# Kernel tuning notes

Hardware: AMD Instinct MI355X
Metric: run time of the kernel (lower is better)

## Reference

```python
import jax, jax.numpy as jnp
import numpy as np

B, T, C = 4, 2048, 1024
NUM_HEADS, HEAD_DIM = 16, 64
INNER = NUM_HEADS * HEAD_DIM
OUT_DIM = 1024


def setup_inputs() -> dict:
    key = jax.random.key(0)
    kx, kk, kq, kv, kp = jax.random.split(key, 5)
    return {
        "x": jax.random.normal(kx, (B, T, C), dtype=jnp.float32),
        "W_k": jax.random.normal(kk, (INNER, C), dtype=jnp.float32),
        "W_q": jax.random.normal(kq, (INNER, C), dtype=jnp.float32),
        "W_v": jax.random.normal(kv, (INNER, C), dtype=jnp.float32),
        "W_p": jax.random.normal(kp, (OUT_DIM, INNER), dtype=jnp.float32),
    }


def reference(x, W_k, W_q, W_v, W_p):
    b, t, c = x.shape
    h, d = NUM_HEADS, HEAD_DIM
    scale_in = c ** (-0.5)
    # project and split heads: [B, H, T, D]
    def proj(W):
        y = jnp.einsum('btc,ic->bti', x, W) * scale_in
        return y.reshape(b, t, h, d).transpose(0, 2, 1, 3)
    k = proj(W_k)
    q = proj(W_q)
    v = proj(W_v)
    scores = jnp.einsum('bhqd,bhkd->bhqk', q, k) * (d ** (-0.5))
    weight = jax.nn.softmax(scores, axis=-1)
    out = jnp.einsum('bhqk,bhkd->bhqd', weight, v)  # [B,H,T,D]
    out = out.transpose(0, 2, 1, 3).reshape(b, t, h * d)
    out = jnp.einsum('bti,oi->bto', out, W_p) * (W_p.shape[-1] ** (-0.5))
    return out
```

## Files before the change

kernel.cpp:

```cpp
#include <hip/hip_runtime.h>
#include <math.h>

typedef __attribute__((ext_vector_type(8))) short bh8;
typedef __attribute__((ext_vector_type(4))) float f32x4;

namespace {
constexpr int Bn = 4, Tn = 2048, Cn = 1024, Hn = 16, Dn = 64, INNERn = 1024, OUTn = 1024;
constexpr int Mn = Bn * Tn;
}

__device__ __forceinline__ void glds16(const void* g, void* l) {
    __builtin_amdgcn_global_load_lds(
        (const __attribute__((address_space(1))) void*)g,
        (__attribute__((address_space(3))) void*)l, 16, 0, 0);
}

__device__ __forceinline__ void barrier_vm0() {
    __builtin_amdgcn_s_waitcnt(0x0070);
    __builtin_amdgcn_s_barrier();
}

__device__ __forceinline__ ushort f2bf(float f) {
    union { float f; unsigned u; } v; v.f = f;
    unsigned r = v.u + 0x7fffu + ((v.u >> 16) & 1u);
    return (ushort)(r >> 16);
}
__device__ __forceinline__ unsigned pack_rne(float a, float b) {
    return (unsigned)f2bf(a) | ((unsigned)f2bf(b) << 16);
}
__device__ __forceinline__ unsigned pack_trunc(float a, float b) {
    return __builtin_amdgcn_perm(__float_as_uint(a), __float_as_uint(b), 0x03020706u);
}

__global__ __launch_bounds__(256)
void cvt_all(const float* __restrict__ x,  const float* __restrict__ Wk,
             const float* __restrict__ Wq, const float* __restrict__ Wv,
             const float* __restrict__ Wp,
             ushort* __restrict__ xb,  ushort* __restrict__ wkb,
             ushort* __restrict__ wqb, ushort* __restrict__ wvb,
             ushort* __restrict__ wpb)
{
    const int bid = blockIdx.x;
    const float* s; ushort* d; float sc; int i;
    if (bid < 8192) {
        s = x; d = xb; sc = 0.03125f;
        i = bid * 256 + threadIdx.x;
    } else {
        const int seg = (bid - 8192) >> 10;
        i = ((bid - 8192) & 1023) * 256 + threadIdx.x;
        s  = (seg == 0) ? Wk : (seg == 1) ? Wq : (seg == 2) ? Wv : Wp;
        d  = (seg == 0) ? wkb : (seg == 1) ? wqb : (seg == 2) ? wvb : wpb;
        sc = (seg == 3) ? 0.03125f : 1.0f;
    }
    float4 f = ((const float4*)s)[i];
    ushort4 o;
    o.x = f2bf(f.x * sc); o.y = f2bf(f.y * sc);
    o.z = f2bf(f.z * sc); o.w = f2bf(f.w * sc);
    ((ushort4*)d)[i] = o;
}

__global__ __launch_bounds__(256)
void gemm_qkv(const ushort* __restrict__ A, const ushort* __restrict__ Wq,
              const ushort* __restrict__ Wk, const ushort* __restrict__ Wv,
              ushort* __restrict__ Oq, ushort* __restrict__ Ok,
              ushort* __restrict__ Ovt, float qscale)
{
    __shared__ char As[2][8192];
    __shared__ char Bs[2][8192];
    const int tid = threadIdx.x;
    const int w = tid >> 6, lane = tid & 63, quad = lane >> 4, l = lane & 15;
    const int sel = blockIdx.x >> 3;
    const ushort* Bw = (sel == 0) ? Wq : (sel == 1) ? Wk : Wv;
    const int n0 = (blockIdx.x & 7) * 128, m0 = blockIdx.y * 128;
    const int wm = w >> 1, wn = w & 1;

    auto stage = [&](int bsel, int k0) {
#pragma unroll
        for (int rr = 0; rr < 2; ++rr) {
            const int rho = w * 2 + rr;
            const int row = rho * 16 + (lane >> 2);
            const int kq  = (lane & 3) * 8;
            glds16(A  + (size_t)(m0 + row) * Cn + k0 + kq, As[bsel] + rho * 1024 + lane * 16);
            glds16(Bw + (size_t)(n0 + row) * Cn + k0 + kq, Bs[bsel] + rho * 1024 + lane * 16);
        }
    };

    f32x4 acc[4][4];
#pragma unroll
    for (int i = 0; i < 4; ++i)
#pragma unroll
        for (int j = 0; j < 4; ++j) acc[i][j] = (f32x4){0.f, 0.f, 0.f, 0.f};

    stage(0, 0);
    barrier_vm0();
#pragma unroll 2
    for (int it = 0; it < 32; ++it) {
        const int cur = it & 1;
        if (it < 31) stage(cur ^ 1, (it + 1) * 32);
        const char* Ac = As[cur]; const char* Bc = Bs[cur];
        bh8 af[4], bf[4];
#pragma unroll
        for (int mf = 0; mf < 4; ++mf)
            af[mf] = *(const bh8*)(Ac + (wm * 64 + mf * 16 + l) * 64 + quad * 16);
#pragma unroll
        for (int nf = 0; nf < 4; ++nf)
            bf[nf] = *(const bh8*)(Bc + (wn * 64 + nf * 16 + l) * 64 + quad * 16);
#pragma unroll
        for (int mf = 0; mf < 4; ++mf)
#pragma unroll
            for (int nf = 0; nf < 4; ++nf)
                acc[mf][nf] = __builtin_amdgcn_mfma_f32_16x16x32_bf16(af[mf], bf[nf], acc[mf][nf], 0, 0, 0);
        barrier_vm0();
    }

    if (sel < 2) {
        ushort* dU = (sel == 0) ? Oq : Ok;
        const float scale = (sel == 0) ? qscale : 1.0f;
#pragma unroll
        for (int mf = 0; mf < 4; ++mf)
#pragma unroll
            for (int nf = 0; nf < 4; ++nf) {
                const int mb = m0 + wm * 64 + mf * 16 + quad * 4;
                const int n  = n0 + wn * 64 + nf * 16 + l;
                const int h = n >> 6, dd = n & 63;
#pragma unroll
                for (int reg = 0; reg < 4; ++reg) {
                    const int m = mb + reg;
                    const int b = m >> 11, t = m & (Tn - 1);
                    dU[((size_t)(b * Hn + h) * Tn + t) * Dn + dd] = f2bf(acc[mf][nf][reg] * scale);
                }
            }
    } else {
#pragma unroll
        for (int mf = 0; mf < 4; ++mf)
#pragma unroll
            for (int nf = 0; nf < 4; ++nf) {
                const int mb = m0 + wm * 64 + mf * 16 + quad * 4;
                const int n  = n0 + wn * 64 + nf * 16 + l;
                const int h = n >> 6, dd = n & 63;
                const int b = mb >> 11, t0 = mb & (Tn - 1);
                uint2 p;
                p.x = pack_rne(acc[mf][nf][0], acc[mf][nf][1]);
                p.y = pack_rne(acc[mf][nf][2], acc[mf][nf][3]);
                *(uint2*)(Ovt + ((size_t)(b * Hn + h) * Dn + dd) * Tn + t0) = p;
            }
    }
}

__global__ __launch_bounds__(256)
void gemm_po(const ushort* __restrict__ A, const ushort* __restrict__ Bw,
             float* __restrict__ Cout)
{
    __shared__ char As[2][8192];
    __shared__ char Bs[2][8192];
    const int tid = threadIdx.x;
    const int w = tid >> 6, lane = tid & 63, quad = lane >> 4, l = lane & 15;
    const int n0 = blockIdx.x * 128, m0 = blockIdx.y * 128;
    const int wm = w >> 1, wn = w & 1;

    auto stage = [&](int bsel, int k0) {
#pragma unroll
        for (int rr = 0; rr < 2; ++rr) {
            const int rho = w * 2 + rr;
            const int row = rho * 16 + (lane >> 2);
            const int kq  = (lane & 3) * 8;
            glds16(A  + (size_t)(m0 + row) * Cn + k0 + kq, As[bsel] + rho * 1024 + lane * 16);
            glds16(Bw + (size_t)(n0 + row) * Cn + k0 + kq, Bs[bsel] + rho * 1024 + lane * 16);
        }
    };

    f32x4 acc[4][4];
#pragma unroll
    for (int i = 0; i < 4; ++i)
#pragma unroll
        for (int j = 0; j < 4; ++j) acc[i][j] = (f32x4){0.f, 0.f, 0.f, 0.f};

    stage(0, 0);
    barrier_vm0();
#pragma unroll 2
    for (int it = 0; it < 32; ++it) {
        const int cur = it & 1;
        if (it < 31) stage(cur ^ 1, (it + 1) * 32);
        const char* Ac = As[cur]; const char* Bc = Bs[cur];
        bh8 af[4], bf[4];
#pragma unroll
        for (int mf = 0; mf < 4; ++mf)
            af[mf] = *(const bh8*)(Ac + (wm * 64 + mf * 16 + l) * 64 + quad * 16);
#pragma unroll
        for (int nf = 0; nf < 4; ++nf)
            bf[nf] = *(const bh8*)(Bc + (wn * 64 + nf * 16 + l) * 64 + quad * 16);
#pragma unroll
        for (int mf = 0; mf < 4; ++mf)
#pragma unroll
            for (int nf = 0; nf < 4; ++nf)
                acc[mf][nf] = __builtin_amdgcn_mfma_f32_16x16x32_bf16(af[mf], bf[nf], acc[mf][nf], 0, 0, 0);
        barrier_vm0();
    }

#pragma unroll
    for (int mf = 0; mf < 4; ++mf)
#pragma unroll
        for (int nf = 0; nf < 4; ++nf) {
            const int mb = m0 + wm * 64 + mf * 16 + quad * 4;
            const int n  = n0 + wn * 64 + nf * 16 + l;
#pragma unroll
            for (int reg = 0; reg < 4; ++reg)
                Cout[(size_t)(mb + reg) * OUTn + n] = acc[mf][nf][reg];
        }
}

__global__ __launch_bounds__(256, 2)
void attn_mfma(const ushort* __restrict__ Qg, const ushort* __restrict__ Kg,
               const ushort* __restrict__ Vtg, ushort* __restrict__ Og)
{
    __shared__ char KT[2][8192];
    __shared__ char VT[2][8192];
    __shared__ char PS[16384];

    const int tid = threadIdx.x;
    const int w = tid >> 6, lane = tid & 63, quad = lane >> 4, l = lane & 15;
    const int q0 = blockIdx.x * 256;
    const int bh = blockIdx.y, b = bh >> 4, h = bh & 15;
    const ushort* Qp = Qg  + (size_t)bh * Tn * Dn;
    const ushort* Kp = Kg  + (size_t)bh * Tn * Dn;
    const ushort* Vp = Vtg + (size_t)bh * Dn * Tn;

    auto stageK = [&](char* buf, int kt) {
#pragma unroll
        for (int rr = 0; rr < 2; ++rr) {
            const int rho = w * 2 + rr;
            const int r  = (rho & 3) * 16 + (lane >> 2);
            const int dq = (rho >> 2) * 32 + (lane & 3) * 8;
            glds16(Kp + (size_t)(kt * 64 + r) * Dn + dq, buf + rho * 1024 + lane * 16);
        }
    };
    auto stageV = [&](char* buf, int kt) {
#pragma unroll
        for (int rr = 0; rr < 2; ++rr) {
            const int rho = w * 2 + rr;
            const int d = rho * 8 + (lane >> 3);
            const int csrc = (lane & 7) ^ ((lane >> 3) & 7);
            glds16(Vp + (size_t)d * Tn + kt * 64 + csrc * 8, buf + rho * 1024 + lane * 16);
        }
    };

    bh8 qf[4][2];
#pragma unroll
    for (int nt = 0; nt < 4; ++nt)
#pragma unroll
        for (int ks = 0; ks < 2; ++ks)
            qf[nt][ks] = *(const bh8*)(Qp + (size_t)(q0 + w * 64 + nt * 16 + l) * Dn + ks * 32 + quad * 8);

    bh8 ones;
#pragma unroll
    for (int i = 0; i < 8; ++i) ones[i] = (short)0x3F80;

    f32x4 oacc[4][4], lacc[4];
#pragma unroll
    for (int nt = 0; nt < 4; ++nt) {
        lacc[nt] = (f32x4){0.f, 0.f, 0.f, 0.f};
#pragma unroll
        for (int dt = 0; dt < 4; ++dt) oacc[nt][dt] = (f32x4){0.f, 0.f, 0.f, 0.f};
    }

    char* Pw = PS + w * 4096;
    const f32x4 zero = (f32x4){0.f, 0.f, 0.f, 0.f};

    stageK(KT[0], 0);
    stageV(VT[0], 0);
    barrier_vm0();

    for (int kt = 0; kt < Tn / 64; ++kt) {
        const int cur = kt & 1;
        if (kt < Tn / 64 - 1) {
            stageK(KT[cur ^ 1], kt + 1);
            stageV(VT[cur ^ 1], kt + 1);
        }
        const char* Kc = KT[cur];
        const char* Vc = VT[cur];

#pragma unroll
        for (int hh = 0; hh < 2; ++hh) {
            bh8 kf[2][2];
#pragma unroll
            for (int k8l = 0; k8l < 2; ++k8l)
#pragma unroll
                for (int ks = 0; ks < 2; ++ks)
                    kf[k8l][ks] = *(const bh8*)(Kc + ks * 4096 + ((hh * 2 + k8l) * 16 + l) * 64 + quad * 16);

            f32x4 st[4][2];
#pragma unroll
            for (int nt = 0; nt < 4; ++nt)
#pragma unroll
                for (int k8l = 0; k8l < 2; ++k8l) {
                    st[nt][k8l] = __builtin_amdgcn_mfma_f32_16x16x32_bf16(kf[k8l][0], qf[nt][0], zero, 0, 0, 0);
                    st[nt][k8l] = __builtin_amdgcn_mfma_f32_16x16x32_bf16(kf[k8l][1], qf[nt][1], st[nt][k8l], 0, 0, 0);
                }

#pragma unroll
            for (int nt = 0; nt < 4; ++nt)
#pragma unroll
                for (int k8l = 0; k8l < 2; ++k8l) {
                    const float e0 = __builtin_amdgcn_exp2f(st[nt][k8l][0]);
                    const float e1 = __builtin_amdgcn_exp2f(st[nt][k8l][1]);
                    const float e2 = __builtin_amdgcn_exp2f(st[nt][k8l][2]);
                    const float e3 = __builtin_amdgcn_exp2f(st[nt][k8l][3]);
                    uint2 p;
                    p.x = pack_trunc(e0, e1);
                    p.y = pack_trunc(e2, e3);
                    const int x = (k8l * 2 + (quad >> 1)) ^ (l & 3);
                    *(uint2*)(Pw + (nt * 16 + l) * 64 + x * 16 + (quad & 1) * 8) = p;
                }
            __builtin_amdgcn_s_waitcnt(0xC07F);

            bh8 pf[4];
#pragma unroll
            for (int nt = 0; nt < 4; ++nt)
                pf[nt] = *(const bh8*)(Pw + (nt * 16 + l) * 64 + ((quad ^ (l & 3)) * 16));
#pragma unroll
            for (int nt = 0; nt < 4; ++nt)
                lacc[nt] = __builtin_amdgcn_mfma_f32_16x16x32_bf16(ones, pf[nt], lacc[nt], 0, 0, 0);
#pragma unroll
            for (int dt = 0; dt < 4; ++dt) {
                bh8 vf = *(const bh8*)(Vc + (dt * 16 + l) * 128 + (((hh * 4 + quad) ^ (l & 7)) * 16));
#pragma unroll
                for (int nt = 0; nt < 4; ++nt)
                    oacc[nt][dt] = __builtin_amdgcn_mfma_f32_16x16x32_bf16(vf, pf[nt], oacc[nt][dt], 0, 0, 0);
            }
        }
        barrier_vm0();
    }

#pragma unroll
    for (int nt = 0; nt < 4; ++nt) {
        const float inv = 1.0f / lacc[nt][0];
        const int t = q0 + w * 64 + nt * 16 + l;
#pragma unroll
        for (int dt = 0; dt < 4; ++dt) {
            uint2 p;
            p.x = pack_rne(oacc[nt][dt][0] * inv, oacc[nt][dt][1] * inv);
            p.y = pack_rne(oacc[nt][dt][2] * inv, oacc[nt][dt][3] * inv);
            *(uint2*)(Og + ((size_t)(b * Tn + t)) * INNERn + h * 64 + dt * 16 + quad * 4) = p;
        }
    }
}

extern "C" void kernel_launch(void* const* d_in, const int* in_sizes, int n_in,
                              void* d_out, int out_size, void* d_ws, size_t ws_size,
                              hipStream_t stream)
{
    const float* x  = (const float*)d_in[0];
    const float* Wk = (const float*)d_in[1];
    const float* Wq = (const float*)d_in[2];
    const float* Wv = (const float*)d_in[3];
    const float* Wp = (const float*)d_in[4];
    float* out = (float*)d_out;

    ushort* xb  = (ushort*)d_ws;
    ushort* wkb = xb  + (size_t)Mn * Cn;
    ushort* wqb = wkb + (size_t)INNERn * Cn;
    ushort* wvb = wqb + (size_t)INNERn * Cn;
    ushort* wpb = wvb + (size_t)INNERn * Cn;
    ushort* qw  = wpb + (size_t)OUTn * INNERn;
    ushort* kw  = qw  + (size_t)Mn * INNERn;
    ushort* vtw = kw  + (size_t)Mn * INNERn;
    ushort* aow = vtw + (size_t)Mn * INNERn;

    const dim3 blk(256);
    cvt_all<<<dim3(8192 + 4096), blk, 0, stream>>>(x, Wk, Wq, Wv, Wp,
                                                   xb, wkb, wqb, wvb, wpb);

    gemm_qkv<<<dim3(3 * 8, Mn / 128), blk, 0, stream>>>(xb, wqb, wkb, wvb,
                                                        qw, kw, vtw, 0.125f * 1.44269504f);

    attn_mfma<<<dim3(Tn / 256, Bn * Hn), blk, 0, stream>>>(qw, kw, vtw, aow);

    gemm_po<<<dim3(OUTn / 128, Mn / 128), blk, 0, stream>>>(aow, wpb, out);
}
```

Before: 290.8 us.

## Halve attention query tile for higher occupancy; stage V^T output through LDS

The attention kernel now processes 128 queries per block instead of 256 (32 per wave), halving per-wave accumulators and the P scratch buffer so four blocks can fit per CU, with twice as many blocks launched. Each block still streams the full K/V sequence, so total K/V traffic doubles. Separately, the QKV GEMM writes the transposed V tile into a swizzled shared-memory buffer and then emits 16-byte coalesced rows, replacing the scattered 8-byte transposed stores.

```diff
diff --git a/kernel.cpp b/kernel.cpp
--- a/kernel.cpp
+++ b/kernel.cpp
@@ -65,13 +65,107 @@
               ushort* __restrict__ Oq, ushort* __restrict__ Ok,
               ushort* __restrict__ Ovt, float qscale)
 {
-    __shared__ char As[2][8192];
-    __shared__ char Bs[2][8192];
+    __shared__ char SM[32768];
+    char* As0 = SM;          char* As1 = SM + 8192;
+    char* Bs0 = SM + 16384;  char* Bs1 = SM + 24576;
     const int tid = threadIdx.x;
     const int w = tid >> 6, lane = tid & 63, quad = lane >> 4, l = lane & 15;
     const int sel = blockIdx.x >> 3;
     const ushort* Bw = (sel == 0) ? Wq : (sel == 1) ? Wk : Wv;
     const int n0 = (blockIdx.x & 7) * 128, m0 = blockIdx.y * 128;
+    const int wm = w >> 1, wn = w & 1;
+
+    auto stage = [&](char* Ad, char* Bd, int k0) {
+#pragma unroll
+        for (int rr = 0; rr < 2; ++rr) {
+            const int rho = w * 2 + rr;
+            const int row = rho * 16 + (lane >> 2);
+            const int kq  = (lane & 3) * 8;
+            glds16(A  + (size_t)(m0 + row) * Cn + k0 + kq, Ad + rho * 1024 + lane * 16);
+            glds16(Bw + (size_t)(n0 + row) * Cn + k0 + kq, Bd + rho * 1024 + lane * 16);
+        }
+    };
+
+    f32x4 acc[4][4];
+#pragma unroll
+    for (int i = 0; i < 4; ++i)
+#pragma unroll
+        for (int j = 0; j < 4; ++j) acc[i][j] = (f32x4){0.f, 0.f, 0.f, 0.f};
+
+    stage(As0, Bs0, 0);
+    barrier_vm0();
+#pragma unroll 2
+    for (int it = 0; it < 32; ++it) {
+        const int cur = it & 1;
+        if (it < 31) stage(cur ? As0 : As1, cur ? Bs0 : Bs1, (it + 1) * 32);
+        const char* Ac = cur ? As1 : As0; const char* Bc = cur ? Bs1 : Bs0;
+        bh8 af[4], bf[4];
+#pragma unroll
+        for (int mf = 0; mf < 4; ++mf)
+            af[mf] = *(const bh8*)(Ac + (wm * 64 + mf * 16 + l) * 64 + quad * 16);
+#pragma unroll
+        for (int nf = 0; nf < 4; ++nf)
+            bf[nf] = *(const bh8*)(Bc + (wn * 64 + nf * 16 + l) * 64 + quad * 16);
+#pragma unroll
+        for (int mf = 0; mf < 4; ++mf)
+#pragma unroll
+            for (int nf = 0; nf < 4; ++nf)
+                acc[mf][nf] = __builtin_amdgcn_mfma_f32_16x16x32_bf16(af[mf], bf[nf], acc[mf][nf], 0, 0, 0);
+        barrier_vm0();
+    }
+
+    if (sel < 2) {
+        ushort* dU = (sel == 0) ? Oq : Ok;
+        const float scale = (sel == 0) ? qscale : 1.0f;
+#pragma unroll
+        for (int mf = 0; mf < 4; ++mf)
+#pragma unroll
+            for (int nf = 0; nf < 4; ++nf) {
+                const int mb = m0 + wm * 64 + mf * 16 + quad * 4;
+                const int n  = n0 + wn * 64 + nf * 16 + l;
+                const int h = n >> 6, dd = n & 63;
+#pragma unroll
+                for (int reg = 0; reg < 4; ++reg) {
+                    const int m = mb + reg;
+                    const int b = m >> 11, t = m & (Tn - 1);
+                    dU[((size_t)(b * Hn + h) * Tn + t) * Dn + dd] = f2bf(acc[mf][nf][reg] * scale);
+                }
+            }
+    } else {
+#pragma unroll
+        for (int mf = 0; mf < 4; ++mf)
+#pragma unroll
+            for (int nf = 0; nf < 4; ++nf) {
+                const int mb = wm * 64 + mf * 16 + quad * 4;
+                const int n  = wn * 64 + nf * 16 + l;
+                uint2 p;
+                p.x = pack_rne(acc[mf][nf][0], acc[mf][nf][1]);
+                p.y = pack_rne(acc[mf][nf][2], acc[mf][nf][3]);
+                const int c = mb >> 3;
+                *(uint2*)(SM + n * 256 + ((c ^ (n & 15)) & 15) * 16 + (mb & 7) * 2) = p;
+            }
+        __syncthreads();
+        const int bb = m0 >> 11, t0 = m0 & (Tn - 1);
+#pragma unroll
+        for (int it2 = 0; it2 < 8; ++it2) {
+            const int n = it2 * 16 + w * 4 + quad;
+            const int ng = n0 + n;
+            const int h = ng >> 6, dd = ng & 63;
+            int4 vsm = *(const int4*)(SM + n * 256 + ((l ^ (n & 15)) & 15) * 16);
+            *(int4*)(Ovt + ((size_t)(bb * Hn + h) * Dn + dd) * Tn + t0 + l * 8) = vsm;
+        }
+    }
+}
+
+__global__ __launch_bounds__(256)
+void gemm_po(const ushort* __restrict__ A, const ushort* __restrict__ Bw,
+             float* __restrict__ Cout)
+{
+    __shared__ char As[2][8192];
+    __shared__ char Bs[2][8192];
+    const int tid = threadIdx.x;
+    const int w = tid >> 6, lane = tid & 63, quad = lane >> 4, l = lane & 15;
+    const int n0 = blockIdx.x * 128, m0 = blockIdx.y * 128;
     const int wm = w >> 1, wn = w & 1;
 
     auto stage = [&](int bsel, int k0) {
@@ -113,90 +207,6 @@
         barrier_vm0();
     }
 
-    if (sel < 2) {
-        ushort* dU = (sel == 0) ? Oq : Ok;
-        const float scale = (sel == 0) ? qscale : 1.0f;
-#pragma unroll
-        for (int mf = 0; mf < 4; ++mf)
-#pragma unroll
-            for (int nf = 0; nf < 4; ++nf) {
-                const int mb = m0 + wm * 64 + mf * 16 + quad * 4;
-                const int n  = n0 + wn * 64 + nf * 16 + l;
-                const int h = n >> 6, dd = n & 63;
-#pragma unroll
-                for (int reg = 0; reg < 4; ++reg) {
-                    const int m = mb + reg;
-                    const int b = m >> 11, t = m & (Tn - 1);
-                    dU[((size_t)(b * Hn + h) * Tn + t) * Dn + dd] = f2bf(acc[mf][nf][reg] * scale);
-                }
-            }
-    } else {
-#pragma unroll
-        for (int mf = 0; mf < 4; ++mf)
-#pragma unroll
-            for (int nf = 0; nf < 4; ++nf) {
-                const int mb = m0 + wm * 64 + mf * 16 + quad * 4;
-                const int n  = n0 + wn * 64 + nf * 16 + l;
-                const int h = n >> 6, dd = n & 63;
-                const int b = mb >> 11, t0 = mb & (Tn - 1);
-                uint2 p;
-                p.x = pack_rne(acc[mf][nf][0], acc[mf][nf][1]);
-                p.y = pack_rne(acc[mf][nf][2], acc[mf][nf][3]);
-                *(uint2*)(Ovt + ((size_t)(b * Hn + h) * Dn + dd) * Tn + t0) = p;
-            }
-    }
-}
-
-__global__ __launch_bounds__(256)
-void gemm_po(const ushort* __restrict__ A, const ushort* __restrict__ Bw,
-             float* __restrict__ Cout)
-{
-    __shared__ char As[2][8192];
-    __shared__ char Bs[2][8192];
-    const int tid = threadIdx.x;
-    const int w = tid >> 6, lane = tid & 63, quad = lane >> 4, l = lane & 15;
-    const int n0 = blockIdx.x * 128, m0 = blockIdx.y * 128;
-    const int wm = w >> 1, wn = w & 1;
-
-    auto stage = [&](int bsel, int k0) {
-#pragma unroll
-        for (int rr = 0; rr < 2; ++rr) {
-            const int rho = w * 2 + rr;
-            const int row = rho * 16 + (lane >> 2);
-            const int kq  = (lane & 3) * 8;
-            glds16(A  + (size_t)(m0 + row) * Cn + k0 + kq, As[bsel] + rho * 1024 + lane * 16);
-            glds16(Bw + (size_t)(n0 + row) * Cn + k0 + kq, Bs[bsel] + rho * 1024 + lane * 16);
-        }
-    };
-
-    f32x4 acc[4][4];
-#pragma unroll
-    for (int i = 0; i < 4; ++i)
-#pragma unroll
-        for (int j = 0; j < 4; ++j) acc[i][j] = (f32x4){0.f, 0.f, 0.f, 0.f};
-
-    stage(0, 0);
-    barrier_vm0();
-#pragma unroll 2
-    for (int it = 0; it < 32; ++it) {
-        const int cur = it & 1;
-        if (it < 31) stage(cur ^ 1, (it + 1) * 32);
-        const char* Ac = As[cur]; const char* Bc = Bs[cur];
-        bh8 af[4], bf[4];
-#pragma unroll
-        for (int mf = 0; mf < 4; ++mf)
-            af[mf] = *(const bh8*)(Ac + (wm * 64 + mf * 16 + l) * 64 + quad * 16);
-#pragma unroll
-        for (int nf = 0; nf < 4; ++nf)
-            bf[nf] = *(const bh8*)(Bc + (wn * 64 + nf * 16 + l) * 64 + quad * 16);
-#pragma unroll
-        for (int mf = 0; mf < 4; ++mf)
-#pragma unroll
-            for (int nf = 0; nf < 4; ++nf)
-                acc[mf][nf] = __builtin_amdgcn_mfma_f32_16x16x32_bf16(af[mf], bf[nf], acc[mf][nf], 0, 0, 0);
-        barrier_vm0();
-    }
-
 #pragma unroll
     for (int mf = 0; mf < 4; ++mf)
 #pragma unroll
@@ -209,17 +219,17 @@
         }
 }
 
-__global__ __launch_bounds__(256, 2)
+__global__ __launch_bounds__(256, 4)
 void attn_mfma(const ushort* __restrict__ Qg, const ushort* __restrict__ Kg,
                const ushort* __restrict__ Vtg, ushort* __restrict__ Og)
 {
     __shared__ char KT[2][8192];
     __shared__ char VT[2][8192];
-    __shared__ char PS[16384];
+    __shared__ char PS[8192];
 
     const int tid = threadIdx.x;
     const int w = tid >> 6, lane = tid & 63, quad = lane >> 4, l = lane & 15;
-    const int q0 = blockIdx.x * 256;
+    const int q0 = blockIdx.x * 128;
     const int bh = blockIdx.y, b = bh >> 4, h = bh & 15;
     const ushort* Qp = Qg  + (size_t)bh * Tn * Dn;
     const ushort* Kp = Kg  + (size_t)bh * Tn * Dn;
@@ -244,32 +254,33 @@
         }
     };
 
-    bh8 qf[4][2];
-#pragma unroll
-    for (int nt = 0; nt < 4; ++nt)
+    bh8 qf[2][2];
+#pragma unroll
+    for (int nt = 0; nt < 2; ++nt)
 #pragma unroll
         for (int ks = 0; ks < 2; ++ks)
-            qf[nt][ks] = *(const bh8*)(Qp + (size_t)(q0 + w * 64 + nt * 16 + l) * Dn + ks * 32 + quad * 8);
+            qf[nt][ks] = *(const bh8*)(Qp + (size_t)(q0 + w * 32 + nt * 16 + l) * Dn + ks * 32 + quad * 8);
 
     bh8 ones;
 #pragma unroll
     for (int i = 0; i < 8; ++i) ones[i] = (short)0x3F80;
 
-    f32x4 oacc[4][4], lacc[4];
-#pragma unroll
-    for (int nt = 0; nt < 4; ++nt) {
+    f32x4 oacc[2][4], lacc[2];
+#pragma unroll
+    for (int nt = 0; nt < 2; ++nt) {
         lacc[nt] = (f32x4){0.f, 0.f, 0.f, 0.f};
 #pragma unroll
         for (int dt = 0; dt < 4; ++dt) oacc[nt][dt] = (f32x4){0.f, 0.f, 0.f, 0.f};
     }
 
-    char* Pw = PS + w * 4096;
+    char* Pw = PS + w * 2048;
     const f32x4 zero = (f32x4){0.f, 0.f, 0.f, 0.f};
 
     stageK(KT[0], 0);
     stageV(VT[0], 0);
     barrier_vm0();
 
+#pragma unroll 2
     for (int kt = 0; kt < Tn / 64; ++kt) {
         const int cur = kt & 1;
         if (kt < Tn / 64 - 1) {
@@ -288,9 +299,9 @@
                 for (int ks = 0; ks < 2; ++ks)
                     kf[k8l][ks] = *(const bh8*)(Kc + ks * 4096 + ((hh * 2 + k8l) * 16 + l) * 64 + quad * 16);
 
-            f32x4 st[4][2];
-#pragma unroll
-            for (int nt = 0; nt < 4; ++nt)
+            f32x4 st[2][2];
+#pragma unroll
+            for (int nt = 0; nt < 2; ++nt)
 #pragma unroll
                 for (int k8l = 0; k8l < 2; ++k8l) {
                     st[nt][k8l] = __builtin_amdgcn_mfma_f32_16x16x32_bf16(kf[k8l][0], qf[nt][0], zero, 0, 0, 0);
@@ -298,7 +309,7 @@
                 }
 
 #pragma unroll
-            for (int nt = 0; nt < 4; ++nt)
+            for (int nt = 0; nt < 2; ++nt)
 #pragma unroll
                 for (int k8l = 0; k8l < 2; ++k8l) {
                     const float e0 = __builtin_amdgcn_exp2f(st[nt][k8l][0]);
@@ -313,18 +324,18 @@
                 }
             __builtin_amdgcn_s_waitcnt(0xC07F);
 
-            bh8 pf[4];
-#pragma unroll
-            for (int nt = 0; nt < 4; ++nt)
+            bh8 pf[2];
+#pragma unroll
+            for (int nt = 0; nt < 2; ++nt)
                 pf[nt] = *(const bh8*)(Pw + (nt * 16 + l) * 64 + ((quad ^ (l & 3)) * 16));
 #pragma unroll
-            for (int nt = 0; nt < 4; ++nt)
+            for (int nt = 0; nt < 2; ++nt)
                 lacc[nt] = __builtin_amdgcn_mfma_f32_16x16x32_bf16(ones, pf[nt], lacc[nt], 0, 0, 0);
 #pragma unroll
             for (int dt = 0; dt < 4; ++dt) {
                 bh8 vf = *(const bh8*)(Vc + (dt * 16 + l) * 128 + (((hh * 4 + quad) ^ (l & 7)) * 16));
 #pragma unroll
-                for (int nt = 0; nt < 4; ++nt)
+                for (int nt = 0; nt < 2; ++nt)
                     oacc[nt][dt] = __builtin_amdgcn_mfma_f32_16x16x32_bf16(vf, pf[nt], oacc[nt][dt], 0, 0, 0);
             }
         }
@@ -332,9 +343,9 @@
     }
 
 #pragma unroll
-    for (int nt = 0; nt < 4; ++nt) {
+    for (int nt = 0; nt < 2; ++nt) {
         const float inv = 1.0f / lacc[nt][0];
-        const int t = q0 + w * 64 + nt * 16 + l;
+        const int t = q0 + w * 32 + nt * 16 + l;
 #pragma unroll
         for (int dt = 0; dt < 4; ++dt) {
             uint2 p;
@@ -373,7 +384,7 @@
     gemm_qkv<<<dim3(3 * 8, Mn / 128), blk, 0, stream>>>(xb, wqb, wkb, wvb,
                                                         qw, kw, vtw, 0.125f * 1.44269504f);
 
-    attn_mfma<<<dim3(Tn / 256, Bn * Hn), blk, 0, stream>>>(qw, kw, vtw, aow);
+    attn_mfma<<<dim3(Tn / 128, Bn * Hn), blk, 0, stream>>>(qw, kw, vtw, aow);
 
     gemm_po<<<dim3(OUTn / 128, Mn / 128), blk, 0, stream>>>(aow, wpb, out);
 }
```

Result: faster. 283.4 us (-2.5%).
